# Kernel tuning notes

Measured on AMD Instinct MI355X. Metric: run time of the kernel, lower is better.

Reference implementation:

```python
import jax, jax.numpy as jnp
import numpy as np

BN_EPS = 1e-5

# Binary_a: sign forward, hard-tanh STE backward (grad zeroed where |x| >= 1)
@jax.custom_vjp
def binary_act(x):
    return jnp.sign(x)

def _ba_fwd(x):
    return jnp.sign(x), x

def _ba_bwd(x, g):
    return (jnp.where((x > -1.0) & (x < 1.0), g, 0.0),)

binary_act.defvjp(_ba_fwd, _ba_bwd)

# Binary_w: sign forward, identity STE backward
@jax.custom_vjp
def binary_w(x):
    return jnp.sign(x)

def _bw_fwd(x):
    return jnp.sign(x), None

def _bw_bwd(_, g):
    return (g,)

binary_w.defvjp(_bw_fwd, _bw_bwd)


def setup_inputs() -> dict:
    key = jax.random.key(0)
    k1, k2, k3 = jax.random.split(key, 3)
    B, Cin, Cout, H, Wd, K = 32, 256, 256, 56, 56, 3
    x = jax.random.normal(k1, (B, Cin, H, Wd), dtype=jnp.float32)
    weight = jax.random.normal(k2, (Cout, Cin, K, K), dtype=jnp.float32) * 0.05
    bias = jax.random.normal(k3, (Cout,), dtype=jnp.float32) * 0.01
    gamma = jnp.ones((Cout,), dtype=jnp.float32)
    beta = jnp.zeros((Cout,), dtype=jnp.float32)
    return {"x": x, "weight": weight, "bias": bias, "gamma": gamma, "beta": beta}


def reference(x, weight, bias, gamma, beta):
    # activation binarization (A=2)
    xb = binary_act(x)
    # weight quantization (W=2): mean-center over in-channel dim, clamp to [-1,1]
    # (done on .data in torch -> values change but no grad through this step)
    wc_val = jnp.clip(weight - jnp.mean(weight, axis=1, keepdims=True), -1.0, 1.0)
    wc = weight + jax.lax.stop_gradient(wc_val - weight)
    # per-output-filter scale alpha = E[|w|] over (in, kh, kw)
    alpha = jnp.mean(jnp.abs(wc), axis=(1, 2, 3), keepdims=True)
    wq = binary_w(wc) * alpha  # [O,I,K,K]
    # conv2d, stride 1, padding 1, groups 1
    y = jax.lax.conv_general_dilated(
        xb, wq, window_strides=(1, 1), padding=((1, 1), (1, 1)),
        dimension_numbers=("NCHW", "OIHW", "NCHW"))
    y = y + bias[None, :, None, None]
    # BatchNorm2d, training-mode forward (biased batch stats)
    mean = jnp.mean(y, axis=(0, 2, 3), keepdims=True)
    var = jnp.mean(jnp.square(y - mean), axis=(0, 2, 3), keepdims=True)
    y = (y - mean) * jax.lax.rsqrt(var + BN_EPS)
    y = y * gamma[None, :, None, None] + beta[None, :, None, None]
    # last_relu=1
    return jax.nn.relu(y)
```

## Files before the change

kernel.cpp:

```cpp
#include <hip/hip_runtime.h>
#include <stdint.h>

typedef unsigned long long u64;
typedef unsigned int u32;
typedef int v4i __attribute__((ext_vector_type(4)));
typedef int v16i __attribute__((ext_vector_type(16)));

#define B_    32
#define CIN   256
#define COUT  256
#define H_    56
#define W_    56
#define HW    3136
#define NPOS  100352
#define NROW  1792
#define NPACKBLK 784


__global__ __launch_bounds__(256) void k_prep(
    const float* __restrict__ x,
    const float* __restrict__ wgt,
    u64* __restrict__ xbits,
    int8_t* __restrict__ Bfrag,
    float* __restrict__ alpha,
    int* __restrict__ ssum,
    unsigned long long* __restrict__ qsum)
{
    const int tid = threadIdx.x;

    if (blockIdx.x < NPACKBLK) {
        const int j = blockIdx.x / 196;
        const int p2 = (blockIdx.x - j * 196) * 256 + tid;
        const int pos0 = p2 * 2;
        const int b = pos0 / HW;
        const int hw = pos0 - b * HW;
        const float* xp = x + (size_t)b * CIN * HW + (size_t)j * 64 * HW + hw;
        u64 b0 = 0, b1 = 0;
#pragma unroll 8
        for (int k = 0; k < 64; ++k) {
            const float2 v = *(const float2*)(xp + (size_t)k * HW);
            b0 |= (u64)(v.x > 0.0f) << k;
            b1 |= (u64)(v.y > 0.0f) << k;
        }
        xbits[(size_t)pos0 * 4 + j] = b0;
        xbits[(size_t)(pos0 + 1) * 4 + j] = b1;
        return;
    }

    const int o = blockIdx.x - NPACKBLK;
    const int i = tid;
    const int wave = i >> 6, lane = i & 63;
    __shared__ float sred[4][12];

    if (i == 0) { ssum[o] = 0; qsum[o] = 0ULL; }

    float w9[9];
#pragma unroll
    for (int t = 0; t < 9; ++t) w9[t] = wgt[(o * 256 + i) * 9 + t];

    float m[9];
#pragma unroll
    for (int t = 0; t < 9; ++t) m[t] = w9[t];
#pragma unroll
    for (int s = 1; s < 64; s <<= 1)
#pragma unroll
        for (int t = 0; t < 9; ++t) m[t] += __shfl_xor(m[t], s, 64);
    if (lane == 0) {
#pragma unroll
        for (int t = 0; t < 9; ++t) sred[wave][t] = m[t];
    }
    __syncthreads();
#pragma unroll
    for (int t = 0; t < 9; ++t)
        m[t] = (sred[0][t] + sred[1][t] + sred[2][t] + sred[3][t]) * (1.0f / 256.0f);

    float wc[9];
    float asum = 0.0f;
#pragma unroll
    for (int t = 0; t < 9; ++t) {
        float v = w9[t] - m[t];
        v = fminf(fmaxf(v, -1.0f), 1.0f);
        wc[t] = v;
        asum += fabsf(v);
    }
#pragma unroll
    for (int s = 1; s < 64; s <<= 1) asum += __shfl_xor(asum, s, 64);
    __syncthreads();
    if (lane == 0) sred[wave][9] = asum;
    __syncthreads();
    if (i == 0)
        alpha[o] = (sred[0][9] + sred[1][9] + sred[2][9] + sred[3][9]) * (1.0f / 2304.0f);

#pragma unroll
    for (int t = 0; t < 9; ++t) {
        const int8_t sv = (wc[t] > 0.0f) ? (int8_t)1 : (int8_t)-1;
        const size_t addr =
            ((size_t)((t * 8 + (i >> 5)) * 8 + (o >> 5)) * 64
             + (size_t)(((i >> 4) & 1) * 32 + (o & 31))) * 16 + (i & 15);
        Bfrag[addr] = sv;
    }
}

#define MFMA_I8(acc, a, b) \
    asm volatile("v_mfma_i32_32x32x32_i8 %0, %1, %2, %0" : "+a"(acc) : "v"(a), "v"(b))

__global__ __launch_bounds__(256, 3) void kc_mfma(
    const u64* __restrict__ xbits,
    const int8_t* __restrict__ Bfrag,
    short* __restrict__ S,
    int* __restrict__ ssum,
    unsigned long long* __restrict__ qsum)
{
    const int blk = blockIdx.x;
    const int b = blk / H_;
    const int h = blk - b * H_;
    const int tid = threadIdx.x;

    __shared__ u32 ldsb[3 * 58 * 64];

    for (int it = tid; it < 3 * 58 * 16; it += 256) {
        const int r = it / 928;
        const int rem = it - r * 928;
        const int wp = rem >> 4;
        const int g = rem & 15;
        const int hr = h - 1 + r;
        const int w_in = wp - 1;
        const bool inb = (hr >= 0) && (hr < H_) && (w_in >= 0) && (w_in < W_);
        u32 chunk16 = 0;
        if (inb) {
            const u64 word = xbits[((size_t)(b * HW + hr * W_ + w_in)) * 4 + (g >> 2)];
            chunk16 = (u32)(word >> ((g & 3) * 16)) & 0xFFFFu;
        }
        u32 out4[4];
#pragma unroll
        for (int d = 0; d < 4; ++d) {
            const u32 nib = (chunk16 >> (4 * d)) & 0xFu;
            const u32 m1 = (nib * 0x00204081u) & 0x01010101u;
            const u32 inv = m1 ^ 0x01010101u;
            out4[d] = inb ? (0x01010101u ^ (inv * 0xFEu)) : 0u;
        }
        const int gs = (g + wp) & 15;
        u32* dst = &ldsb[((r * 58 + wp) << 6) + gs * 4];
        dst[0] = out4[0]; dst[1] = out4[1]; dst[2] = out4[2]; dst[3] = out4[3];
    }
    __syncthreads();

    const int m0 = tid & 31;
    const int lh = (tid >> 5) & 1;
    const int wv = tid >> 6;
    const int8_t* smem = (const int8_t*)ldsb;
    const int8_t* Bp = Bfrag + (size_t)(tid & 63) * 16;

    auto ldA = [&](int kk, int mt) -> v4i {
        const int tap = kk >> 3, s = kk & 7;
        const int dh = tap / 3;
        const int dw = tap - dh * 3;
        const int wpm = min(mt * 32 + m0 + dw, 57);
        const int gs = (2 * s + lh + wpm) & 15;
        const int addr = ((dh * 58 + wpm) << 8) + (gs << 4);
        return *(const v4i*)(smem + addr);
    };
    auto ldB = [&](int kk, int ntl) -> v4i {
        const size_t off = (size_t)((kk * 8) + wv * 2 + ntl) * 1024;
        return *(const v4i*)(Bp + off);
    };

    v16i acc00 = {0}, acc01 = {0}, acc10 = {0}, acc11 = {0};
    v4i A0[2], A1[2], Bb0[2], Bb1[2];

    A0[0] = ldA(0, 0); A1[0] = ldA(0, 1);
    Bb0[0] = ldB(0, 0); Bb1[0] = ldB(0, 1);

#pragma unroll
    for (int kk = 0; kk < 72; ++kk) {
        const int cur = kk & 1, nxt = cur ^ 1;
        if (kk < 71) {
            A0[nxt] = ldA(kk + 1, 0); A1[nxt] = ldA(kk + 1, 1);
            Bb0[nxt] = ldB(kk + 1, 0); Bb1[nxt] = ldB(kk + 1, 1);
        }
        MFMA_I8(acc00, A0[cur], Bb0[cur]);
        MFMA_I8(acc01, A0[cur], Bb1[cur]);
        MFMA_I8(acc10, A1[cur], Bb0[cur]);
        MFMA_I8(acc11, A1[cur], Bb1[cur]);
    }

    asm volatile("s_nop 7\n\ts_nop 7\n\ts_nop 7"
                 : "+a"(acc00), "+a"(acc01), "+a"(acc10), "+a"(acc11));

    const int n0 = wv * 64 + m0;
    const int n1 = n0 + 32;
    const int rowbase = b * HW + h * W_;
    int s0 = 0, s1 = 0, q0 = 0, q1 = 0;

#pragma unroll
    for (int reg = 0; reg < 16; ++reg) {
        const int m = (reg & 3) + ((reg >> 2) << 3) + (lh << 2);
        const int v0 = acc00[reg], v1 = acc01[reg];
        s0 += v0; q0 += v0 * v0; s1 += v1; q1 += v1 * v1;
        S[(size_t)(rowbase + m) * 256 + n0] = (short)v0;
        S[(size_t)(rowbase + m) * 256 + n1] = (short)v1;
    }
#pragma unroll
    for (int reg = 0; reg < 12; ++reg) {
        const int m = 32 + (reg & 3) + ((reg >> 2) << 3) + (lh << 2);
        const int v0 = acc10[reg], v1 = acc11[reg];
        s0 += v0; q0 += v0 * v0; s1 += v1; q1 += v1 * v1;
        S[(size_t)(rowbase + m) * 256 + n0] = (short)v0;
        S[(size_t)(rowbase + m) * 256 + n1] = (short)v1;
    }

    s0 += __shfl_xor(s0, 32, 64); q0 += __shfl_xor(q0, 32, 64);
    s1 += __shfl_xor(s1, 32, 64); q1 += __shfl_xor(q1, 32, 64);
    if (lh == 0) {
        atomicAdd(&ssum[n0], s0);
        atomicAdd(&qsum[n0], (unsigned long long)(long long)q0);
        atomicAdd(&ssum[n1], s1);
        atomicAdd(&qsum[n1], (unsigned long long)(long long)q1);
    }
}

__global__ __launch_bounds__(256) void kb_apply(
    const short* __restrict__ S,
    const int* __restrict__ ssum,
    const unsigned long long* __restrict__ qsum,
    const float* __restrict__ alpha,
    const float* __restrict__ gamma,
    const float* __restrict__ beta,
    float* __restrict__ out)
{
    const int blk = blockIdx.x;
    const int chunk = blk % 49;
    const int bcg = blk / 49;
    const int cg = bcg & 3;
    const int b = bcg >> 2;
    const int c0 = cg * 64;
    const int p0 = chunk * 64;
    const int tid = threadIdx.x;

    __shared__ float s_scale[64], s_shift[64];
    __shared__ u32 lds[64 * 33];

    if (tid < 64) {
        const int o = c0 + tid;
        const double N = (double)NPOS;
        double meanS = (double)ssum[o] / N;
        double varS = (double)qsum[o] / N - meanS * meanS;
        double a = (double)alpha[o];
        double rstd = 1.0 / sqrt(a * a * varS + 1e-5);
        double g = (double)gamma[o];
        s_scale[tid] = (float)(g * a * rstd);
        s_shift[tid] = (float)((double)beta[o] - g * a * meanS * rstd);
    }

    const u32* Sp = (const u32*)(S + ((size_t)b * HW + p0) * 256 + c0);
#pragma unroll
    for (int k = 0; k < 8; ++k) {
        const int idx = tid + k * 256;
        const int p = idx >> 5, cp = idx & 31;
        lds[p * 33 + cp] = Sp[p * 128 + cp];
    }
    __syncthreads();

    const int pl = tid & 63;
    const int ch4 = tid >> 6;
    const short* lss = (const short*)lds;
#pragma unroll
    for (int cc = 0; cc < 16; ++cc) {
        const int c = ch4 * 16 + cc;
        const float f = fmaxf(fmaf((float)lss[pl * 66 + c], s_scale[c], s_shift[c]), 0.0f);
        out[((size_t)(b * COUT + c0 + c)) * HW + p0 + pl] = f;
    }
}

extern "C" void kernel_launch(void* const* d_in, const int* in_sizes, int n_in,
                              void* d_out, int out_size, void* d_ws, size_t ws_size,
                              hipStream_t stream) {
    const float* x     = (const float*)d_in[0];
    const float* wgt   = (const float*)d_in[1];
    const float* gamma = (const float*)d_in[3];
    const float* beta  = (const float*)d_in[4];
    float* out = (float*)d_out;

    char* ws = (char*)d_ws;
    int8_t* Bfrag = (int8_t*)(ws + 0);
    float* alpha = (float*)(ws + 589824);
    int*   ssum  = (int*)(ws + 590848);
    unsigned long long* qsum = (unsigned long long*)(ws + 591872);
    u64*   xbits = (u64*)(ws + 593920);
    short* Sarr  = (short*)(ws + 3805184);

    k_prep<<<NPACKBLK + 256, 256, 0, stream>>>(x, wgt, xbits, Bfrag, alpha, ssum, qsum);
    kc_mfma<<<NROW, 256, 0, stream>>>(xbits, Bfrag, Sarr, ssum, qsum);
    kb_apply<<<32 * 4 * 49, 256, 0, stream>>>(Sarr, ssum, qsum, alpha, gamma, beta, out);
}
```

Measured before the change: 279.2 us.

## Compute two output rows per block to reuse weight fragments and halo rows

Each conv block now handles two output image rows instead of one, loading a 4-row halo into LDS and running 8 MFMA accumulators (4 M-tiles x 2 N-tiles) per wave. Every B-fragment load from global memory now feeds twice as many MFMAs, and the overlapping input rows are packed once instead of twice. The grid is halved and the occupancy hint drops from 3 to 2 blocks per CU. The extra accumulators raise register pressure, and the smaller grid gives fewer waves to hide latency.

```diff
diff --git a/kernel.cpp b/kernel.cpp
--- a/kernel.cpp
+++ b/kernel.cpp
@@ -13,7 +13,7 @@
 #define W_    56
 #define HW    3136
 #define NPOS  100352
-#define NROW  1792
+#define HBLK  28
 #define NPACKBLK 784
 
 
@@ -104,7 +104,7 @@
 #define MFMA_I8(acc, a, b) \
     asm volatile("v_mfma_i32_32x32x32_i8 %0, %1, %2, %0" : "+a"(acc) : "v"(a), "v"(b))
 
-__global__ __launch_bounds__(256, 3) void kc_mfma(
+__global__ __launch_bounds__(256, 2) void kc_mfma(
     const u64* __restrict__ xbits,
     const int8_t* __restrict__ Bfrag,
     short* __restrict__ S,
@@ -112,18 +112,18 @@
     unsigned long long* __restrict__ qsum)
 {
     const int blk = blockIdx.x;
-    const int b = blk / H_;
-    const int h = blk - b * H_;
+    const int b = blk / HBLK;
+    const int h0 = (blk - b * HBLK) * 2;
     const int tid = threadIdx.x;
 
-    __shared__ u32 ldsb[3 * 58 * 64];
-
-    for (int it = tid; it < 3 * 58 * 16; it += 256) {
+    __shared__ u32 ldsb[4 * 58 * 64];
+
+    for (int it = tid; it < 4 * 58 * 16; it += 256) {
         const int r = it / 928;
         const int rem = it - r * 928;
         const int wp = rem >> 4;
         const int g = rem & 15;
-        const int hr = h - 1 + r;
+        const int hr = h0 - 1 + r;
         const int w_in = wp - 1;
         const bool inb = (hr >= 0) && (hr < H_) && (w_in >= 0) && (w_in < W_);
         u32 chunk16 = 0;
@@ -155,9 +155,10 @@
         const int tap = kk >> 3, s = kk & 7;
         const int dh = tap / 3;
         const int dw = tap - dh * 3;
-        const int wpm = min(mt * 32 + m0 + dw, 57);
+        const int r = (mt >> 1) + dh;
+        const int wpm = min((mt & 1) * 32 + m0 + dw, 57);
         const int gs = (2 * s + lh + wpm) & 15;
-        const int addr = ((dh * 58 + wpm) << 8) + (gs << 4);
+        const int addr = ((r * 58 + wpm) << 8) + (gs << 4);
         return *(const v4i*)(smem + addr);
     };
     auto ldB = [&](int kk, int ntl) -> v4i {
@@ -165,48 +166,51 @@
         return *(const v4i*)(Bp + off);
     };
 
-    v16i acc00 = {0}, acc01 = {0}, acc10 = {0}, acc11 = {0};
-    v4i A0[2], A1[2], Bb0[2], Bb1[2];
-
-    A0[0] = ldA(0, 0); A1[0] = ldA(0, 1);
-    Bb0[0] = ldB(0, 0); Bb1[0] = ldB(0, 1);
+    v16i acc[4][2] = {};
+    v4i A[4][2], Bb[2][2];
+
+#pragma unroll
+    for (int mt = 0; mt < 4; ++mt) A[mt][0] = ldA(0, mt);
+    Bb[0][0] = ldB(0, 0);
+    Bb[1][0] = ldB(0, 1);
 
 #pragma unroll
     for (int kk = 0; kk < 72; ++kk) {
         const int cur = kk & 1, nxt = cur ^ 1;
         if (kk < 71) {
-            A0[nxt] = ldA(kk + 1, 0); A1[nxt] = ldA(kk + 1, 1);
-            Bb0[nxt] = ldB(kk + 1, 0); Bb1[nxt] = ldB(kk + 1, 1);
-        }
-        MFMA_I8(acc00, A0[cur], Bb0[cur]);
-        MFMA_I8(acc01, A0[cur], Bb1[cur]);
-        MFMA_I8(acc10, A1[cur], Bb0[cur]);
-        MFMA_I8(acc11, A1[cur], Bb1[cur]);
+#pragma unroll
+            for (int mt = 0; mt < 4; ++mt) A[mt][nxt] = ldA(kk + 1, mt);
+            Bb[0][nxt] = ldB(kk + 1, 0);
+            Bb[1][nxt] = ldB(kk + 1, 1);
+        }
+#pragma unroll
+        for (int mt = 0; mt < 4; ++mt) {
+            MFMA_I8(acc[mt][0], A[mt][cur], Bb[0][cur]);
+            MFMA_I8(acc[mt][1], A[mt][cur], Bb[1][cur]);
+        }
     }
 
     asm volatile("s_nop 7\n\ts_nop 7\n\ts_nop 7"
-                 : "+a"(acc00), "+a"(acc01), "+a"(acc10), "+a"(acc11));
+                 : "+a"(acc[0][0]), "+a"(acc[0][1]), "+a"(acc[1][0]), "+a"(acc[1][1]),
+                   "+a"(acc[2][0]), "+a"(acc[2][1]), "+a"(acc[3][0]), "+a"(acc[3][1]));
 
     const int n0 = wv * 64 + m0;
     const int n1 = n0 + 32;
-    const int rowbase = b * HW + h * W_;
     int s0 = 0, s1 = 0, q0 = 0, q1 = 0;
 
 #pragma unroll
-    for (int reg = 0; reg < 16; ++reg) {
-        const int m = (reg & 3) + ((reg >> 2) << 3) + (lh << 2);
-        const int v0 = acc00[reg], v1 = acc01[reg];
-        s0 += v0; q0 += v0 * v0; s1 += v1; q1 += v1 * v1;
-        S[(size_t)(rowbase + m) * 256 + n0] = (short)v0;
-        S[(size_t)(rowbase + m) * 256 + n1] = (short)v1;
-    }
-#pragma unroll
-    for (int reg = 0; reg < 12; ++reg) {
-        const int m = 32 + (reg & 3) + ((reg >> 2) << 3) + (lh << 2);
-        const int v0 = acc10[reg], v1 = acc11[reg];
-        s0 += v0; q0 += v0 * v0; s1 += v1; q1 += v1 * v1;
-        S[(size_t)(rowbase + m) * 256 + n0] = (short)v0;
-        S[(size_t)(rowbase + m) * 256 + n1] = (short)v1;
+    for (int mt = 0; mt < 4; ++mt) {
+        const int h = h0 + (mt >> 1);
+        const int rowbase = b * HW + h * W_ + ((mt & 1) << 5);
+        const int nval = (mt & 1) ? 12 : 16;
+#pragma unroll 16
+        for (int reg = 0; reg < nval; ++reg) {
+            const int m = (reg & 3) + ((reg >> 2) << 3) + (lh << 2);
+            const int v0 = acc[mt][0][reg], v1 = acc[mt][1][reg];
+            s0 += v0; q0 += v0 * v0; s1 += v1; q1 += v1 * v1;
+            S[(size_t)(rowbase + m) * 256 + n0] = (short)v0;
+            S[(size_t)(rowbase + m) * 256 + n1] = (short)v1;
+        }
     }
 
     s0 += __shfl_xor(s0, 32, 64); q0 += __shfl_xor(q0, 32, 64);
@@ -290,6 +294,6 @@
     short* Sarr  = (short*)(ws + 3805184);
 
     k_prep<<<NPACKBLK + 256, 256, 0, stream>>>(x, wgt, xbits, Bfrag, alpha, ssum, qsum);
-    kc_mfma<<<NROW, 256, 0, stream>>>(xbits, Bfrag, Sarr, ssum, qsum);
+    kc_mfma<<<B_ * HBLK, 256, 0, stream>>>(xbits, Bfrag, Sarr, ssum, qsum);
     kb_apply<<<32 * 4 * 49, 256, 0, stream>>>(Sarr, ssum, qsum, alpha, gamma, beta, out);
 }
```

After: 279.5 us. About the same (+0.1%).
